# Kernel optimization log

Hardware: AMD Instinct MI355X
Metric: run time of the kernel (lower is better)

## Reference

```python
import jax, jax.numpy as jnp
import numpy as np

N_NODES = 100000

def gcn_conv(x, W, b, src, dst):
    # PyG GCNConv: h = x @ W; add self-loops; symmetric norm D^-1/2 A D^-1/2; scatter-add; + bias
    n = x.shape[0]
    h = x @ W  # transform first (out_dim small) -> cheap messages
    loop = jnp.arange(n, dtype=src.dtype)
    s = jnp.concatenate([src, loop])
    d = jnp.concatenate([dst, loop])
    deg = jax.ops.segment_sum(jnp.ones_like(d, dtype=h.dtype), d, num_segments=n)
    dinv = jnp.where(deg > 0, jax.lax.rsqrt(deg), 0.0)
    norm = dinv[s] * dinv[d]  # [E+N]
    msg = h[s] * norm[:, None]  # gather + scale
    out = jax.ops.segment_sum(msg, d, num_segments=n)  # scatter-add to targets
    return out + b

def setup_inputs() -> dict:
    key = jax.random.key(0)
    k1, k2, k3, k4 = jax.random.split(key, 4)
    x = jax.random.normal(k1, (N_NODES, 128), dtype=jnp.float32)
    edge_index = jax.random.randint(k2, (2, 3200000), 0, N_NODES, dtype=jnp.int64)
    W1 = jax.random.normal(k3, (128, 16), dtype=jnp.float32) * 0.1
    b1 = jnp.zeros((16,), dtype=jnp.float32)
    W2 = jax.random.normal(k4, (16, 7), dtype=jnp.float32) * 0.1
    b2 = jnp.zeros((7,), dtype=jnp.float32)
    return {"x": x, "edge_index": edge_index, "W1": W1, "b1": b1, "W2": W2, "b2": b2}

def reference(x, edge_index, W1, b1, W2, b2):
    src, dst = edge_index[0], edge_index[1]
    h = gcn_conv(x, W1, b1, src, dst)
    h = jax.nn.relu(h)
    # F.dropout(training=self.training) is identity in eval mode
    h = gcn_conv(h, W2, b2, src, dst)
    return jax.nn.log_softmax(h, axis=1)
```

## Files before the change

### kernel.cpp

```cpp
#include <hip/hip_runtime.h>
#include <hip/hip_bf16.h>
#include <math.h>


#define FIN 128
#define FMID 16
#define FOUT 7

#define LBITS 7
#define NPB   128
#define SBITS 17
#define SMASK 0x1FFFF
#define NB_MAX 800
#define CAP   5120
#define EPT   12
#define BINT  1024
#define TILE  (EPT * BINT)

#define G1N   128
#define AS1   20
#define AS2   12

__global__ void zero_kernel(int* __restrict__ p, int m) {
    int i = blockIdx.x * 256 + threadIdx.x;
    if (i < m) p[i] = 0;
}

__global__ __launch_bounds__(BINT) void bin_kernel(const int* __restrict__ src,
                                                   const int* __restrict__ dst,
                                                   int* __restrict__ pairs,
                                                   int* __restrict__ gcnt,
                                                   int e, int nb) {
    __shared__ int sorted[TILE];
    __shared__ int cnt[NB_MAX], excl[NB_MAX], lofs[NB_MAX], gbase[NB_MAX];
    __shared__ int wsum[16];
    int tid = threadIdx.x;
    for (int j = tid; j < nb; j += BINT) cnt[j] = 0;
    __syncthreads();

    int base = blockIdx.x * TILE;
    int w[EPT], bk[EPT];
#pragma unroll
    for (int k = 0; k < EPT; ++k) {
        int idx = base + k * BINT + tid;
        if (idx < e) {
            int d = dst[idx], s = src[idx];
            w[k]  = ((d & (NPB - 1)) << SBITS) | s;
            bk[k] = d >> LBITS;
            atomicAdd(&cnt[bk[k]], 1);
        } else bk[k] = -1;
    }
    __syncthreads();

    if (tid < nb && cnt[tid] > 0) gbase[tid] = atomicAdd(&gcnt[tid], cnt[tid]);

    {
        int v = (tid < nb) ? cnt[tid] : 0;
        int lane = tid & 63, wid = tid >> 6;
        int incl = v;
#pragma unroll
        for (int d = 1; d < 64; d <<= 1) {
            int t = __shfl_up(incl, d);
            if (lane >= d) incl += t;
        }
        if (lane == 63) wsum[wid] = incl;
        __syncthreads();
        if (tid < 16) {
            int wv = wsum[tid];
            int wincl = wv;
#pragma unroll
            for (int d = 1; d < 16; d <<= 1) {
                int t = __shfl_up(wincl, d);
                if (tid >= d) wincl += t;
            }
            wsum[tid] = wincl - wv;
        }
        __syncthreads();
        if (tid < nb) {
            int ex = wsum[wid] + incl - v;
            excl[tid] = ex;
            lofs[tid] = ex;
        }
    }
    __syncthreads();

#pragma unroll
    for (int k = 0; k < EPT; ++k) {
        if (bk[k] >= 0) {
            int pos = atomicAdd(&lofs[bk[k]], 1);
            sorted[pos] = w[k];
        }
    }
    __syncthreads();

    int g16 = tid >> 4, l16 = tid & 15;
    for (int j = g16; j < nb; j += 64) {
        int c = cnt[j];
        if (!c) continue;
        int st = excl[j], gb = gbase[j];
        size_t go = (size_t)j * CAP;
        for (int l = l16; l < c; l += 16)
            if (gb + l < CAP) pairs[go + gb + l] = sorted[st + l];
    }
}

__global__ __launch_bounds__(512) void sort_kernel(int* __restrict__ pairs,
                                                   const int* __restrict__ gcnt,
                                                   int* __restrict__ rs_g,
                                                   float* __restrict__ dinv, int n) {
    __shared__ int praw[CAP];
    __shared__ int slist[CAP];
    __shared__ int cnt[NPB], rowstart[NPB], lofs[NPB];
    int tid = threadIdx.x, b = blockIdx.x;
    if (tid < NPB) cnt[tid] = 0;
    __syncthreads();

    int c = min(gcnt[b], CAP);
    size_t go = (size_t)b * CAP;

    for (int i = tid; i < c; i += 512) {
        int w = pairs[go + i];
        praw[i] = w;
        atomicAdd(&cnt[w >> SBITS], 1);
    }
    __syncthreads();

    int v = 0, incl = 0;
    __shared__ int wtot_s;
    if (tid < NPB) {
        v = cnt[tid];
        incl = v;
        int lane = tid & 63;
#pragma unroll
        for (int d = 1; d < 64; d <<= 1) {
            int t = __shfl_up(incl, d);
            if (lane >= d) incl += t;
        }
        if (tid == 63) wtot_s = incl;
    }
    __syncthreads();
    if (tid < NPB) {
        int ex = incl - v + ((tid >= 64) ? wtot_s : 0);
        rowstart[tid] = ex;
        lofs[tid] = ex;
    }
    __syncthreads();

    for (int i = tid; i < c; i += 512) {
        int w = praw[i];
        int pos = atomicAdd(&lofs[w >> SBITS], 1);
        slist[pos] = w & SMASK;
    }
    __syncthreads();

    for (int i = tid; i < c; i += 512) pairs[go + i] = slist[i];
    if (tid < NPB) {
        rs_g[b * NPB + tid] = rowstart[tid];
        int node = b * NPB + tid;
        if (node < n) dinv[node] = rsqrtf((float)cnt[tid] + 1.0f);
    }
}

__global__ __launch_bounds__(256) void gemm1_kernel(const float* __restrict__ x,
                                                    const float* __restrict__ W,
                                                    const float* __restrict__ dinv,
                                                    float* __restrict__ h1, int n,
                                                    int sentinel) {
    __shared__ float WsT[16 * 132];
    int tid = threadIdx.x;
    int n0 = blockIdx.x * G1N;

    for (int i = tid; i < FIN * FMID; i += 256) {
        int k = i >> 4, f = i & 15;
        WsT[f * 132 + k] = W[i];
    }
    __syncthreads();

    int ngrp = tid >> 3;
    int f = tid & 7;
    int r0 = n0 + ngrp, r1 = r0 + 32, r2 = r0 + 64, r3 = r0 + 96;
    int nc = n - 1;
    size_t c0 = (size_t)min(r0, nc) * 32;
    size_t c1 = (size_t)min(r1, nc) * 32;
    size_t c2 = (size_t)min(r2, nc) * 32;
    size_t c3 = (size_t)min(r3, nc) * 32;

    const float4* x4  = (const float4*)x;
    const float4* wa4 = (const float4*)(WsT + f * 132);
    const float4* wb4 = (const float4*)(WsT + (f + 8) * 132);

    float a0 = 0.f, a1 = 0.f, a2 = 0.f, a3 = 0.f;
    float b0 = 0.f, b1_ = 0.f, b2_ = 0.f, b3 = 0.f;

#pragma unroll 8
    for (int ck = 0; ck < 32; ++ck) {
        float4 x0 = x4[c0 + ck];
        float4 x1 = x4[c1 + ck];
        float4 x2 = x4[c2 + ck];
        float4 x3 = x4[c3 + ck];
        float4 wa = wa4[ck];
        float4 wb = wb4[ck];
        a0 += x0.x * wa.x + x0.y * wa.y + x0.z * wa.z + x0.w * wa.w;
        a1 += x1.x * wa.x + x1.y * wa.y + x1.z * wa.z + x1.w * wa.w;
        a2 += x2.x * wa.x + x2.y * wa.y + x2.z * wa.z + x2.w * wa.w;
        a3 += x3.x * wa.x + x3.y * wa.y + x3.z * wa.z + x3.w * wa.w;
        b0  += x0.x * wb.x + x0.y * wb.y + x0.z * wb.z + x0.w * wb.w;
        b1_ += x1.x * wb.x + x1.y * wb.y + x1.z * wb.z + x1.w * wb.w;
        b2_ += x2.x * wb.x + x2.y * wb.y + x2.z * wb.z + x2.w * wb.w;
        b3  += x3.x * wb.x + x3.y * wb.y + x3.z * wb.z + x3.w * wb.w;
    }

    float ra[4] = {a0, a1, a2, a3};
    float rb[4] = {b0, b1_, b2_, b3};
    int rr[4] = {r0, r1, r2, r3};
#pragma unroll
    for (int i = 0; i < 4; ++i) {
        int node = rr[i];
        if (node < n) {
            float dd = dinv ? dinv[node] : 1.0f;
            h1[(size_t)node * FMID + f]     = ra[i] * dd;
            h1[(size_t)node * FMID + f + 8] = rb[i] * dd;
        } else if (node == n && sentinel) {
            h1[(size_t)n * FMID + f]     = 0.0f;
            h1[(size_t)n * FMID + f + 8] = 0.0f;
        }
    }
}

__global__ __launch_bounds__(512) void scatter1_kernel(const int* __restrict__ pairs,
                                                       const int* __restrict__ gcnt,
                                                       const int* __restrict__ rs_g,
                                                       const float* __restrict__ dinv,
                                                       const float* __restrict__ h1s,
                                                       const float* __restrict__ b1,
                                                       const float* __restrict__ W2,
                                                       float* __restrict__ h3s, int n) {
    __shared__ int   slist[CAP + 8];
    __shared__ int   rowstart_s[NPB + 1];
    __shared__ float acc2[NPB * AS1];
    __shared__ float W2s[FMID * FOUT];
    __shared__ float b1s[FMID];
    int tid = threadIdx.x, b = blockIdx.x;
    int c = min(gcnt[b], CAP);
    size_t go = (size_t)b * CAP;

    if (tid < FMID * FOUT) W2s[tid] = W2[tid];
    if (tid < FMID) b1s[tid] = b1[tid];
    if (tid < NPB) rowstart_s[tid] = rs_g[b * NPB + tid];
    if (tid == 0) rowstart_s[NPB] = c;
    for (int i = tid; i < c; i += 512) slist[i] = pairs[go + i];
    __syncthreads();

    {
        int nd = tid >> 2, q = tid & 3;
        int pbeg = rowstart_s[nd];
        int pend = rowstart_s[nd + 1];
        const float4* h4 = (const float4*)h1s;
        float4 acc = make_float4(0.f, 0.f, 0.f, 0.f);
        for (int p = pbeg; p < pend; p += 8) {
            int i0 = (p + 0 < pend) ? slist[p + 0] : n;
            int i1 = (p + 1 < pend) ? slist[p + 1] : n;
            int i2 = (p + 2 < pend) ? slist[p + 2] : n;
            int i3 = (p + 3 < pend) ? slist[p + 3] : n;
            int i4 = (p + 4 < pend) ? slist[p + 4] : n;
            int i5 = (p + 5 < pend) ? slist[p + 5] : n;
            int i6 = (p + 6 < pend) ? slist[p + 6] : n;
            int i7 = (p + 7 < pend) ? slist[p + 7] : n;
            float4 v0 = h4[(size_t)i0 * 4 + q];
            float4 v1 = h4[(size_t)i1 * 4 + q];
            float4 v2 = h4[(size_t)i2 * 4 + q];
            float4 v3 = h4[(size_t)i3 * 4 + q];
            float4 v4 = h4[(size_t)i4 * 4 + q];
            float4 v5 = h4[(size_t)i5 * 4 + q];
            float4 v6 = h4[(size_t)i6 * 4 + q];
            float4 v7 = h4[(size_t)i7 * 4 + q];
            acc.x += v0.x; acc.y += v0.y; acc.z += v0.z; acc.w += v0.w;
            acc.x += v1.x; acc.y += v1.y; acc.z += v1.z; acc.w += v1.w;
            acc.x += v2.x; acc.y += v2.y; acc.z += v2.z; acc.w += v2.w;
            acc.x += v3.x; acc.y += v3.y; acc.z += v3.z; acc.w += v3.w;
            acc.x += v4.x; acc.y += v4.y; acc.z += v4.z; acc.w += v4.w;
            acc.x += v5.x; acc.y += v5.y; acc.z += v5.z; acc.w += v5.w;
            acc.x += v6.x; acc.y += v6.y; acc.z += v6.z; acc.w += v6.w;
            acc.x += v7.x; acc.y += v7.y; acc.z += v7.z; acc.w += v7.w;
        }
        float* a = acc2 + nd * AS1 + q * 4;
        a[0] = acc.x; a[1] = acc.y; a[2] = acc.z; a[3] = acc.w;
    }
    __syncthreads();

    int node = b * NPB + tid;
    if (tid < NPB && node < n) {
        float dd = dinv[node];
        float vbuf[FMID];
#pragma unroll
        for (int k = 0; k < FMID; ++k) {
            float t = dd * (acc2[tid * AS1 + k] + h1s[(size_t)node * FMID + k]) + b1s[k];
            vbuf[k] = t > 0.0f ? t : 0.0f;
        }
        float sj[8];
#pragma unroll
        for (int j = 0; j < FOUT; ++j) {
            float s = 0.0f;
#pragma unroll
            for (int k = 0; k < FMID; ++k) s += vbuf[k] * W2s[k * FOUT + j];
            sj[j] = s * dd;
        }
        sj[7] = 0.0f;
        float4* o4 = (float4*)(h3s + (size_t)node * 8);
        o4[0] = make_float4(sj[0], sj[1], sj[2], sj[3]);
        o4[1] = make_float4(sj[4], sj[5], sj[6], 0.0f);
    } else if (tid < NPB && node == n) {
        float4* o4 = (float4*)(h3s + (size_t)n * 8);
        o4[0] = make_float4(0.f, 0.f, 0.f, 0.f);
        o4[1] = make_float4(0.f, 0.f, 0.f, 0.f);
    }
}

__global__ __launch_bounds__(512) void scatter2_kernel(const int* __restrict__ pairs,
                                                       const int* __restrict__ gcnt,
                                                       const int* __restrict__ rs_g,
                                                       const float* __restrict__ dinv,
                                                       const float* __restrict__ h3s,
                                                       const float* __restrict__ b2,
                                                       float* __restrict__ out, int n) {
    __shared__ int   slist[CAP + 16];
    __shared__ int   rowstart_s[NPB + 1];
    __shared__ float acc2[NPB * AS2];
    __shared__ float b2s[8];
    int tid = threadIdx.x, b = blockIdx.x;
    int c = min(gcnt[b], CAP);
    size_t go = (size_t)b * CAP;

    if (tid < FOUT) b2s[tid] = b2[tid];
    if (tid < NPB) rowstart_s[tid] = rs_g[b * NPB + tid];
    if (tid == 0) rowstart_s[NPB] = c;
    for (int i = tid; i < c; i += 512) slist[i] = pairs[go + i];
    __syncthreads();

    {
        int nd = tid >> 2, l = tid & 3;
        int eo = l >> 1, half = l & 1;
        int pbeg = rowstart_s[nd];
        int pend = rowstart_s[nd + 1];
        const float4* h4 = (const float4*)h3s;
        float4 acc = make_float4(0.f, 0.f, 0.f, 0.f);
        for (int p = pbeg + eo; p < pend; p += 8) {
            int i0 = (p + 0 < pend) ? slist[p + 0] : n;
            int i1 = (p + 2 < pend) ? slist[p + 2] : n;
            int i2 = (p + 4 < pend) ? slist[p + 4] : n;
            int i3 = (p + 6 < pend) ? slist[p + 6] : n;
            float4 v0 = h4[(size_t)i0 * 2 + half];
            float4 v1 = h4[(size_t)i1 * 2 + half];
            float4 v2 = h4[(size_t)i2 * 2 + half];
            float4 v3 = h4[(size_t)i3 * 2 + half];
            acc.x += v0.x; acc.y += v0.y; acc.z += v0.z; acc.w += v0.w;
            acc.x += v1.x; acc.y += v1.y; acc.z += v1.z; acc.w += v1.w;
            acc.x += v2.x; acc.y += v2.y; acc.z += v2.z; acc.w += v2.w;
            acc.x += v3.x; acc.y += v3.y; acc.z += v3.z; acc.w += v3.w;
        }
        acc.x += __shfl_xor(acc.x, 2);
        acc.y += __shfl_xor(acc.y, 2);
        acc.z += __shfl_xor(acc.z, 2);
        acc.w += __shfl_xor(acc.w, 2);
        if (eo == 0) {
            float* a = acc2 + nd * AS2 + half * 4;
            a[0] = acc.x; a[1] = acc.y; a[2] = acc.z; a[3] = acc.w;
        }
    }
    __syncthreads();

    int node = b * NPB + tid;
    if (tid < NPB && node < n) {
        float dd = dinv[node];
        float t[FOUT], m = -INFINITY;
#pragma unroll
        for (int j = 0; j < FOUT; ++j) {
            t[j] = dd * (acc2[tid * AS2 + j] + h3s[(size_t)node * 8 + j]) + b2s[j];
            m = fmaxf(m, t[j]);
        }
        float sum = 0.0f;
#pragma unroll
        for (int j = 0; j < FOUT; ++j) sum += expf(t[j] - m);
        float lse = logf(sum);
#pragma unroll
        for (int j = 0; j < FOUT; ++j) out[(size_t)node * FOUT + j] = t[j] - m - lse;
    }
}

__global__ void fb_deg_kernel(const int* __restrict__ dst, float* __restrict__ deg, int e) {
    int i = blockIdx.x * blockDim.x + threadIdx.x;
    if (i < e) atomicAdd(&deg[dst[i]], 1.0f);
}
__global__ void fb_dinv_kernel(float* __restrict__ deg, int n) {
    int i = blockIdx.x * blockDim.x + threadIdx.x;
    if (i < n) deg[i] = rsqrtf(deg[i] + 1.0f);
}
__global__ void fb_scatter1_kernel(const int* __restrict__ src, const int* __restrict__ dst,
                                   const float* __restrict__ dinv, const float* __restrict__ h1,
                                   float* __restrict__ out1, int e) {
    int i = blockIdx.x * blockDim.x + threadIdx.x;
    if (i >= e) return;
    int s = src[i], d = dst[i];
    float norm = dinv[s] * dinv[d];
    const float4* hs = (const float4*)(h1 + (size_t)s * FMID);
    float* o = out1 + (size_t)d * FMID;
#pragma unroll
    for (int q = 0; q < 4; ++q) {
        float4 vv = hs[q];
        atomicAdd(o + q * 4 + 0, vv.x * norm);
        atomicAdd(o + q * 4 + 1, vv.y * norm);
        atomicAdd(o + q * 4 + 2, vv.z * norm);
        atomicAdd(o + q * 4 + 3, vv.w * norm);
    }
}
__global__ void fb_layer2_kernel(const float* __restrict__ agg, const float* __restrict__ h1,
                                 const float* __restrict__ dinv, const float* __restrict__ b1,
                                 const float* __restrict__ W2, float* __restrict__ h3, int n) {
    int i = blockIdx.x * blockDim.x + threadIdx.x;
    if (i >= n) return;
    float dii = dinv[i] * dinv[i];
    float v[FMID];
#pragma unroll
    for (int k = 0; k < FMID; ++k) {
        float t = agg[(size_t)i * FMID + k] + h1[(size_t)i * FMID + k] * dii + b1[k];
        v[k] = t > 0.0f ? t : 0.0f;
    }
#pragma unroll
    for (int j = 0; j < FOUT; ++j) {
        float s = 0.0f;
#pragma unroll
        for (int k = 0; k < FMID; ++k) s += v[k] * W2[k * FOUT + j];
        h3[(size_t)i * FOUT + j] = s;
    }
}
__global__ void fb_scatter2_kernel(const int* __restrict__ src, const int* __restrict__ dst,
                                   const float* __restrict__ dinv, const float* __restrict__ h3,
                                   float* __restrict__ out2, int e) {
    int i = blockIdx.x * blockDim.x + threadIdx.x;
    if (i >= e) return;
    int s = src[i], d = dst[i];
    float norm = dinv[s] * dinv[d];
    const float* hs = h3 + (size_t)s * FOUT;
    float* o = out2 + (size_t)d * FOUT;
#pragma unroll
    for (int j = 0; j < FOUT; ++j) atomicAdd(o + j, hs[j] * norm);
}
__global__ void fb_finalize_kernel(const float* __restrict__ agg2, const float* __restrict__ h3,
                                   const float* __restrict__ dinv, const float* __restrict__ b2,
                                   float* __restrict__ out, int n) {
    int i = blockIdx.x * blockDim.x + threadIdx.x;
    if (i >= n) return;
    float dii = dinv[i] * dinv[i];
    float t[FOUT], m = -INFINITY;
#pragma unroll
    for (int j = 0; j < FOUT; ++j) {
        t[j] = agg2[(size_t)i * FOUT + j] + h3[(size_t)i * FOUT + j] * dii + b2[j];
        m = fmaxf(m, t[j]);
    }
    float sum = 0.0f;
#pragma unroll
    for (int j = 0; j < FOUT; ++j) sum += expf(t[j] - m);
    float lse = logf(sum);
#pragma unroll
    for (int j = 0; j < FOUT; ++j) out[(size_t)i * FOUT + j] = t[j] - m - lse;
}

extern "C" void kernel_launch(void* const* d_in, const int* in_sizes, int n_in,
                              void* d_out, int out_size, void* d_ws, size_t ws_size,
                              hipStream_t stream) {
    const float* x  = (const float*)d_in[0];
    const int*   ei = (const int*)d_in[1];
    const float* W1 = (const float*)d_in[2];
    const float* b1 = (const float*)d_in[3];
    const float* W2 = (const float*)d_in[4];
    const float* b2 = (const float*)d_in[5];

    const int n = in_sizes[0] / FIN;
    const int e = in_sizes[1] / 2;
    const int* src = ei;
    const int* dst = ei + e;

    const int nb  = (n + NPB - 1) / NPB;
    const int nb2 = (n + 1 + NPB - 1) / NPB;

    size_t need = ((size_t)NB_MAX + (size_t)nb * CAP + (size_t)n +
                   (size_t)nb2 * NPB + (size_t)16 * (n + 1) + (size_t)8 * (n + 1)) * 4;

    if (nb2 <= NB_MAX && n + 1 < (1 << SBITS) && ws_size >= need) {
        int*   gcnt  = (int*)d_ws;
        int*   pairs = gcnt + NB_MAX;
        float* dinv  = (float*)(pairs + (size_t)nb * CAP);
        int*   rs_g  = (int*)(dinv + n);
        float* h1s   = (float*)(rs_g + (size_t)nb2 * NPB);
        float* h3s   = h1s + (size_t)16 * (n + 1);

        zero_kernel<<<(NB_MAX + 255) / 256, 256, 0, stream>>>(gcnt, NB_MAX);

        int gridBin = (e + TILE - 1) / TILE;
        bin_kernel<<<gridBin, BINT, 0, stream>>>(src, dst, pairs, gcnt, e, nb);
        sort_kernel<<<nb, 512, 0, stream>>>(pairs, gcnt, rs_g, dinv, n);
        gemm1_kernel<<<nb2, 256, 0, stream>>>(x, W1, dinv, h1s, n, 1);
        scatter1_kernel<<<nb2, 512, 0, stream>>>(pairs, gcnt, rs_g, dinv, h1s, b1, W2, h3s, n);
        scatter2_kernel<<<nb, 512, 0, stream>>>(pairs, gcnt, rs_g, dinv, h3s, b2, (float*)d_out, n);
    } else {
        float* ws   = (float*)d_ws;
        float* deg  = ws;
        float* out1 = ws + (size_t)n;
        float* out2 = ws + (size_t)17 * n;
        float* h1   = ws + (size_t)24 * n;
        float* h3   = ws + (size_t)40 * n;

        hipMemsetAsync(ws, 0, (size_t)24 * n * sizeof(float), stream);

        const int B = 256;
        const int gridE = (e + B - 1) / B;
        const int gridN = (n + B - 1) / B;
        fb_deg_kernel<<<gridE, B, 0, stream>>>(dst, deg, e);
        fb_dinv_kernel<<<gridN, B, 0, stream>>>(deg, n);
        gemm1_kernel<<<(n + G1N - 1) / G1N, 256, 0, stream>>>(x, W1, nullptr, h1, n, 0);
        fb_scatter1_kernel<<<gridE, B, 0, stream>>>(src, dst, deg, h1, out1, e);
        fb_layer2_kernel<<<gridN, B, 0, stream>>>(out1, h1, deg, b1, W2, h3, n);
        fb_scatter2_kernel<<<gridE, B, 0, stream>>>(src, dst, deg, h3, out2, e);
        fb_finalize_kernel<<<gridN, B, 0, stream>>>(out2, h3, deg, b2, (float*)d_out, n);
    }
}
```

Measured before the change: 120.2 us.

## Store intermediate node features in fp16 to halve gather traffic

The per-node hidden features h1 (16 wide) and h3 (8 wide) are now stored as half precision, so each gathered row in the two scatter passes moves half as many bytes. Both scatter kernels are restructured around this, with new lane-to-edge mappings, fp16-to-fp32 unpacking into float accumulators, and shuffle reductions. The fallback path gets its own simple fp32 GEMM because gemm1 now writes halves. The cost is reduced precision in the stored messages, which could push results outside tolerance.

After: 107.5 us. 1.12x faster.

```diff
diff --git a/kernel.cpp b/kernel.cpp
--- a/kernel.cpp
+++ b/kernel.cpp
@@ -1,5 +1,6 @@
 #include <hip/hip_runtime.h>
 #include <hip/hip_bf16.h>
+#include <hip/hip_fp16.h>
 #include <math.h>
 
 
@@ -18,12 +19,22 @@
 #define TILE  (EPT * BINT)
 
 #define G1N   128
-#define AS1   20
-#define AS2   12
+#define AS1   17
+#define AS2   9
 
 __global__ void zero_kernel(int* __restrict__ p, int m) {
     int i = blockIdx.x * 256 + threadIdx.x;
     if (i < m) p[i] = 0;
+}
+
+__device__ inline void addh8(float* a, float4 v) {
+    const __half2* h = (const __half2*)&v;
+#pragma unroll
+    for (int k = 0; k < 4; ++k) {
+        float2 f = __half22float2(h[k]);
+        a[2 * k]     += f.x;
+        a[2 * k + 1] += f.y;
+    }
 }
 
 __global__ __launch_bounds__(BINT) void bin_kernel(const int* __restrict__ src,
@@ -164,7 +175,7 @@
 __global__ __launch_bounds__(256) void gemm1_kernel(const float* __restrict__ x,
                                                     const float* __restrict__ W,
                                                     const float* __restrict__ dinv,
-                                                    float* __restrict__ h1, int n,
+                                                    __half* __restrict__ h1h, int n,
                                                     int sentinel) {
     __shared__ float WsT[16 * 132];
     int tid = threadIdx.x;
@@ -177,7 +188,7 @@
     __syncthreads();
 
     int ngrp = tid >> 3;
-    int f = tid & 7;
+    int fh = tid & 7;
     int r0 = n0 + ngrp, r1 = r0 + 32, r2 = r0 + 64, r3 = r0 + 96;
     int nc = n - 1;
     size_t c0 = (size_t)min(r0, nc) * 32;
@@ -186,8 +197,8 @@
     size_t c3 = (size_t)min(r3, nc) * 32;
 
     const float4* x4  = (const float4*)x;
-    const float4* wa4 = (const float4*)(WsT + f * 132);
-    const float4* wb4 = (const float4*)(WsT + (f + 8) * 132);
+    const float4* wa4 = (const float4*)(WsT + (2 * fh) * 132);
+    const float4* wb4 = (const float4*)(WsT + (2 * fh + 1) * 132);
 
     float a0 = 0.f, a1 = 0.f, a2 = 0.f, a3 = 0.f;
     float b0 = 0.f, b1_ = 0.f, b2_ = 0.f, b3 = 0.f;
@@ -213,16 +224,15 @@
     float ra[4] = {a0, a1, a2, a3};
     float rb[4] = {b0, b1_, b2_, b3};
     int rr[4] = {r0, r1, r2, r3};
+    __half2* h2 = (__half2*)h1h;
 #pragma unroll
     for (int i = 0; i < 4; ++i) {
         int node = rr[i];
         if (node < n) {
             float dd = dinv ? dinv[node] : 1.0f;
-            h1[(size_t)node * FMID + f]     = ra[i] * dd;
-            h1[(size_t)node * FMID + f + 8] = rb[i] * dd;
+            h2[(size_t)node * 8 + fh] = __floats2half2_rn(ra[i] * dd, rb[i] * dd);
         } else if (node == n && sentinel) {
-            h1[(size_t)n * FMID + f]     = 0.0f;
-            h1[(size_t)n * FMID + f + 8] = 0.0f;
+            h2[(size_t)n * 8 + fh] = __floats2half2_rn(0.0f, 0.0f);
         }
     }
 }
@@ -231,10 +241,10 @@
                                                        const int* __restrict__ gcnt,
                                                        const int* __restrict__ rs_g,
                                                        const float* __restrict__ dinv,
-                                                       const float* __restrict__ h1s,
+                                                       const __half* __restrict__ h1h,
                                                        const float* __restrict__ b1,
                                                        const float* __restrict__ W2,
-                                                       float* __restrict__ h3s, int n) {
+                                                       __half* __restrict__ h3h, int n) {
     __shared__ int   slist[CAP + 8];
     __shared__ int   rowstart_s[NPB + 1];
     __shared__ float acc2[NPB * AS1];
@@ -252,100 +262,16 @@
     __syncthreads();
 
     {
-        int nd = tid >> 2, q = tid & 3;
-        int pbeg = rowstart_s[nd];
-        int pend = rowstart_s[nd + 1];
-        const float4* h4 = (const float4*)h1s;
-        float4 acc = make_float4(0.f, 0.f, 0.f, 0.f);
-        for (int p = pbeg; p < pend; p += 8) {
-            int i0 = (p + 0 < pend) ? slist[p + 0] : n;
-            int i1 = (p + 1 < pend) ? slist[p + 1] : n;
-            int i2 = (p + 2 < pend) ? slist[p + 2] : n;
-            int i3 = (p + 3 < pend) ? slist[p + 3] : n;
-            int i4 = (p + 4 < pend) ? slist[p + 4] : n;
-            int i5 = (p + 5 < pend) ? slist[p + 5] : n;
-            int i6 = (p + 6 < pend) ? slist[p + 6] : n;
-            int i7 = (p + 7 < pend) ? slist[p + 7] : n;
-            float4 v0 = h4[(size_t)i0 * 4 + q];
-            float4 v1 = h4[(size_t)i1 * 4 + q];
-            float4 v2 = h4[(size_t)i2 * 4 + q];
-            float4 v3 = h4[(size_t)i3 * 4 + q];
-            float4 v4 = h4[(size_t)i4 * 4 + q];
-            float4 v5 = h4[(size_t)i5 * 4 + q];
-            float4 v6 = h4[(size_t)i6 * 4 + q];
-            float4 v7 = h4[(size_t)i7 * 4 + q];
-            acc.x += v0.x; acc.y += v0.y; acc.z += v0.z; acc.w += v0.w;
-            acc.x += v1.x; acc.y += v1.y; acc.z += v1.z; acc.w += v1.w;
-            acc.x += v2.x; acc.y += v2.y; acc.z += v2.z; acc.w += v2.w;
-            acc.x += v3.x; acc.y += v3.y; acc.z += v3.z; acc.w += v3.w;
-            acc.x += v4.x; acc.y += v4.y; acc.z += v4.z; acc.w += v4.w;
-            acc.x += v5.x; acc.y += v5.y; acc.z += v5.z; acc.w += v5.w;
-            acc.x += v6.x; acc.y += v6.y; acc.z += v6.z; acc.w += v6.w;
-            acc.x += v7.x; acc.y += v7.y; acc.z += v7.z; acc.w += v7.w;
-        }
-        float* a = acc2 + nd * AS1 + q * 4;
-        a[0] = acc.x; a[1] = acc.y; a[2] = acc.z; a[3] = acc.w;
-    }
-    __syncthreads();
-
-    int node = b * NPB + tid;
-    if (tid < NPB && node < n) {
-        float dd = dinv[node];
-        float vbuf[FMID];
-#pragma unroll
-        for (int k = 0; k < FMID; ++k) {
-            float t = dd * (acc2[tid * AS1 + k] + h1s[(size_t)node * FMID + k]) + b1s[k];
-            vbuf[k] = t > 0.0f ? t : 0.0f;
-        }
-        float sj[8];
-#pragma unroll
-        for (int j = 0; j < FOUT; ++j) {
-            float s = 0.0f;
-#pragma unroll
-            for (int k = 0; k < FMID; ++k) s += vbuf[k] * W2s[k * FOUT + j];
-            sj[j] = s * dd;
-        }
-        sj[7] = 0.0f;
-        float4* o4 = (float4*)(h3s + (size_t)node * 8);
-        o4[0] = make_float4(sj[0], sj[1], sj[2], sj[3]);
-        o4[1] = make_float4(sj[4], sj[5], sj[6], 0.0f);
-    } else if (tid < NPB && node == n) {
-        float4* o4 = (float4*)(h3s + (size_t)n * 8);
-        o4[0] = make_float4(0.f, 0.f, 0.f, 0.f);
-        o4[1] = make_float4(0.f, 0.f, 0.f, 0.f);
-    }
-}
-
-__global__ __launch_bounds__(512) void scatter2_kernel(const int* __restrict__ pairs,
-                                                       const int* __restrict__ gcnt,
-                                                       const int* __restrict__ rs_g,
-                                                       const float* __restrict__ dinv,
-                                                       const float* __restrict__ h3s,
-                                                       const float* __restrict__ b2,
-                                                       float* __restrict__ out, int n) {
-    __shared__ int   slist[CAP + 16];
-    __shared__ int   rowstart_s[NPB + 1];
-    __shared__ float acc2[NPB * AS2];
-    __shared__ float b2s[8];
-    int tid = threadIdx.x, b = blockIdx.x;
-    int c = min(gcnt[b], CAP);
-    size_t go = (size_t)b * CAP;
-
-    if (tid < FOUT) b2s[tid] = b2[tid];
-    if (tid < NPB) rowstart_s[tid] = rs_g[b * NPB + tid];
-    if (tid == 0) rowstart_s[NPB] = c;
-    for (int i = tid; i < c; i += 512) slist[i] = pairs[go + i];
-    __syncthreads();
-
-    {
         int nd = tid >> 2, l = tid & 3;
         int eo = l >> 1, half = l & 1;
         int pbeg = rowstart_s[nd];
         int pend = rowstart_s[nd + 1];
-        const float4* h4 = (const float4*)h3s;
-        float4 acc = make_float4(0.f, 0.f, 0.f, 0.f);
+        const float4* h4 = (const float4*)h1h;
+        float acc[8];
+#pragma unroll
+        for (int k = 0; k < 8; ++k) acc[k] = 0.0f;
         for (int p = pbeg + eo; p < pend; p += 8) {
-            int i0 = (p + 0 < pend) ? slist[p + 0] : n;
+            int i0 = slist[p];
             int i1 = (p + 2 < pend) ? slist[p + 2] : n;
             int i2 = (p + 4 < pend) ? slist[p + 4] : n;
             int i3 = (p + 6 < pend) ? slist[p + 6] : n;
@@ -353,18 +279,17 @@
             float4 v1 = h4[(size_t)i1 * 2 + half];
             float4 v2 = h4[(size_t)i2 * 2 + half];
             float4 v3 = h4[(size_t)i3 * 2 + half];
-            acc.x += v0.x; acc.y += v0.y; acc.z += v0.z; acc.w += v0.w;
-            acc.x += v1.x; acc.y += v1.y; acc.z += v1.z; acc.w += v1.w;
-            acc.x += v2.x; acc.y += v2.y; acc.z += v2.z; acc.w += v2.w;
-            acc.x += v3.x; acc.y += v3.y; acc.z += v3.z; acc.w += v3.w;
-        }
-        acc.x += __shfl_xor(acc.x, 2);
-        acc.y += __shfl_xor(acc.y, 2);
-        acc.z += __shfl_xor(acc.z, 2);
-        acc.w += __shfl_xor(acc.w, 2);
+            addh8(acc, v0);
+            addh8(acc, v1);
+            addh8(acc, v2);
+            addh8(acc, v3);
+        }
+#pragma unroll
+        for (int k = 0; k < 8; ++k) acc[k] += __shfl_xor(acc[k], 2);
         if (eo == 0) {
-            float* a = acc2 + nd * AS2 + half * 4;
-            a[0] = acc.x; a[1] = acc.y; a[2] = acc.z; a[3] = acc.w;
+            float* ap = acc2 + nd * AS1 + half * 8;
+#pragma unroll
+            for (int k = 0; k < 8; ++k) ap[k] = acc[k];
         }
     }
     __syncthreads();
@@ -372,10 +297,103 @@
     int node = b * NPB + tid;
     if (tid < NPB && node < n) {
         float dd = dinv[node];
+        const __half2* hrow = (const __half2*)h1h + (size_t)node * 8;
+        float vbuf[FMID];
+#pragma unroll
+        for (int k = 0; k < 8; ++k) {
+            float2 f2v = __half22float2(hrow[k]);
+            float t0 = dd * (acc2[tid * AS1 + 2 * k]     + f2v.x) + b1s[2 * k];
+            float t1 = dd * (acc2[tid * AS1 + 2 * k + 1] + f2v.y) + b1s[2 * k + 1];
+            vbuf[2 * k]     = t0 > 0.0f ? t0 : 0.0f;
+            vbuf[2 * k + 1] = t1 > 0.0f ? t1 : 0.0f;
+        }
+        float sj[8];
+#pragma unroll
+        for (int j = 0; j < FOUT; ++j) {
+            float s = 0.0f;
+#pragma unroll
+            for (int k = 0; k < FMID; ++k) s += vbuf[k] * W2s[k * FOUT + j];
+            sj[j] = s * dd;
+        }
+        sj[7] = 0.0f;
+        float4 st;
+        __half2* sp = (__half2*)&st;
+        sp[0] = __floats2half2_rn(sj[0], sj[1]);
+        sp[1] = __floats2half2_rn(sj[2], sj[3]);
+        sp[2] = __floats2half2_rn(sj[4], sj[5]);
+        sp[3] = __floats2half2_rn(sj[6], 0.0f);
+        ((float4*)h3h)[node] = st;
+    } else if (tid < NPB && node == n) {
+        float4 st = make_float4(0.f, 0.f, 0.f, 0.f);
+        ((float4*)h3h)[n] = st;
+    }
+}
+
+__global__ __launch_bounds__(512) void scatter2_kernel(const int* __restrict__ pairs,
+                                                       const int* __restrict__ gcnt,
+                                                       const int* __restrict__ rs_g,
+                                                       const float* __restrict__ dinv,
+                                                       const __half* __restrict__ h3h,
+                                                       const float* __restrict__ b2,
+                                                       float* __restrict__ out, int n) {
+    __shared__ int   slist[CAP + 8];
+    __shared__ int   rowstart_s[NPB + 1];
+    __shared__ float acc2[NPB * AS2];
+    __shared__ float b2s[8];
+    int tid = threadIdx.x, b = blockIdx.x;
+    int c = min(gcnt[b], CAP);
+    size_t go = (size_t)b * CAP;
+
+    if (tid < FOUT) b2s[tid] = b2[tid];
+    if (tid < NPB) rowstart_s[tid] = rs_g[b * NPB + tid];
+    if (tid == 0) rowstart_s[NPB] = c;
+    for (int i = tid; i < c; i += 512) slist[i] = pairs[go + i];
+    __syncthreads();
+
+    {
+        int nd = tid >> 2, l = tid & 3;
+        int pbeg = rowstart_s[nd];
+        int pend = rowstart_s[nd + 1];
+        const float4* h4 = (const float4*)h3h;
+        float acc[8];
+#pragma unroll
+        for (int k = 0; k < 8; ++k) acc[k] = 0.0f;
+        for (int p = pbeg + l; p < pend; p += 8) {
+            int i0 = slist[p];
+            int i1 = (p + 4 < pend) ? slist[p + 4] : n;
+            float4 v0 = h4[i0];
+            float4 v1 = h4[i1];
+            addh8(acc, v0);
+            addh8(acc, v1);
+        }
+#pragma unroll
+        for (int k = 0; k < 8; ++k) {
+            acc[k] += __shfl_xor(acc[k], 1);
+            acc[k] += __shfl_xor(acc[k], 2);
+        }
+        if (l == 0) {
+            float* ap = acc2 + nd * AS2;
+#pragma unroll
+            for (int k = 0; k < 8; ++k) ap[k] = acc[k];
+        }
+    }
+    __syncthreads();
+
+    int node = b * NPB + tid;
+    if (tid < NPB && node < n) {
+        float dd = dinv[node];
+        const __half2* hrow = (const __half2*)h3h + (size_t)node * 4;
+        float hself[8];
+#pragma unroll
+        for (int k = 0; k < 4; ++k) {
+            float2 f2v = __half22float2(hrow[k]);
+            hself[2 * k] = f2v.x;
+            hself[2 * k + 1] = f2v.y;
+        }
         float t[FOUT], m = -INFINITY;
 #pragma unroll
         for (int j = 0; j < FOUT; ++j) {
-            t[j] = dd * (acc2[tid * AS2 + j] + h3s[(size_t)node * 8 + j]) + b2s[j];
+            t[j] = dd * (acc2[tid * AS2 + j] + hself[j]) + b2s[j];
             m = fmaxf(m, t[j]);
         }
         float sum = 0.0f;
@@ -387,6 +405,15 @@
     }
 }
 
+__global__ void fb_gemm1_kernel(const float* __restrict__ x, const float* __restrict__ W,
+                                float* __restrict__ h1, int n) {
+    int i = blockIdx.x * blockDim.x + threadIdx.x;
+    if (i >= n * FMID) return;
+    int node = i >> 4, f = i & 15;
+    float s = 0.0f;
+    for (int k = 0; k < FIN; ++k) s += x[(size_t)node * FIN + k] * W[k * FMID + f];
+    h1[i] = s;
+}
 __global__ void fb_deg_kernel(const int* __restrict__ dst, float* __restrict__ deg, int e) {
     int i = blockIdx.x * blockDim.x + threadIdx.x;
     if (i < e) atomicAdd(&deg[dst[i]], 1.0f);
@@ -484,24 +511,24 @@
     const int nb2 = (n + 1 + NPB - 1) / NPB;
 
     size_t need = ((size_t)NB_MAX + (size_t)nb * CAP + (size_t)n +
-                   (size_t)nb2 * NPB + (size_t)16 * (n + 1) + (size_t)8 * (n + 1)) * 4;
+                   (size_t)nb2 * NPB + (size_t)8 * (n + 1) + (size_t)4 * (n + 1)) * 4;
 
     if (nb2 <= NB_MAX && n + 1 < (1 << SBITS) && ws_size >= need) {
-        int*   gcnt  = (int*)d_ws;
-        int*   pairs = gcnt + NB_MAX;
-        float* dinv  = (float*)(pairs + (size_t)nb * CAP);
-        int*   rs_g  = (int*)(dinv + n);
-        float* h1s   = (float*)(rs_g + (size_t)nb2 * NPB);
-        float* h3s   = h1s + (size_t)16 * (n + 1);
+        int*    gcnt  = (int*)d_ws;
+        int*    pairs = gcnt + NB_MAX;
+        float*  dinv  = (float*)(pairs + (size_t)nb * CAP);
+        int*    rs_g  = (int*)(dinv + n);
+        __half* h1h   = (__half*)(rs_g + (size_t)nb2 * NPB);
+        __half* h3h   = h1h + (size_t)16 * (n + 1);
 
         zero_kernel<<<(NB_MAX + 255) / 256, 256, 0, stream>>>(gcnt, NB_MAX);
 
         int gridBin = (e + TILE - 1) / TILE;
         bin_kernel<<<gridBin, BINT, 0, stream>>>(src, dst, pairs, gcnt, e, nb);
         sort_kernel<<<nb, 512, 0, stream>>>(pairs, gcnt, rs_g, dinv, n);
-        gemm1_kernel<<<nb2, 256, 0, stream>>>(x, W1, dinv, h1s, n, 1);
-        scatter1_kernel<<<nb2, 512, 0, stream>>>(pairs, gcnt, rs_g, dinv, h1s, b1, W2, h3s, n);
-        scatter2_kernel<<<nb, 512, 0, stream>>>(pairs, gcnt, rs_g, dinv, h3s, b2, (float*)d_out, n);
+        gemm1_kernel<<<nb2, 256, 0, stream>>>(x, W1, dinv, h1h, n, 1);
+        scatter1_kernel<<<nb2, 512, 0, stream>>>(pairs, gcnt, rs_g, dinv, h1h, b1, W2, h3h, n);
+        scatter2_kernel<<<nb, 512, 0, stream>>>(pairs, gcnt, rs_g, dinv, h3h, b2, (float*)d_out, n);
     } else {
         float* ws   = (float*)d_ws;
         float* deg  = ws;
@@ -517,7 +544,7 @@
         const int gridN = (n + B - 1) / B;
         fb_deg_kernel<<<gridE, B, 0, stream>>>(dst, deg, e);
         fb_dinv_kernel<<<gridN, B, 0, stream>>>(deg, n);
-        gemm1_kernel<<<(n + G1N - 1) / G1N, 256, 0, stream>>>(x, W1, nullptr, h1, n, 0);
+        fb_gemm1_kernel<<<(n * FMID + B - 1) / B, B, 0, stream>>>(x, W1, h1, n);
         fb_scatter1_kernel<<<gridE, B, 0, stream>>>(src, dst, deg, h1, out1, e);
         fb_layer2_kernel<<<gridN, B, 0, stream>>>(out1, h1, deg, b1, W2, h3, n);
         fb_scatter2_kernel<<<gridE, B, 0, stream>>>(src, dst, deg, h3, out2, e);
```
